# Optimization experiments

Hardware: AMD Instinct MI355X
Metric: run time of the kernel (lower is better)

The kernel has to match this reference:

```python
import jax, jax.numpy as jnp
import numpy as np

TOP_K = 48
NUM_RBF = 16
NUM_RBF_SC = 8
MAXREL = 32
EDGE_F = 128
EPS_D = 1e-6
LN_EPS = 1e-5


def gather_nodes(nodes, idx):
    # nodes: [B, L, C], idx: [B, L, K] -> [B, L, K, C]
    return jax.vmap(lambda n, i: n[i])(nodes, idx)


def rbf(D, count):
    # D: [..., ] -> [..., count]; mu in [2, 22], sigma = 20/count
    mu = jnp.linspace(2.0, 22.0, count)
    sigma = (22.0 - 2.0) / count
    return jnp.exp(-(((D[..., None] - mu) / sigma) ** 2))


def layer_norm(x, g, b):
    mu = jnp.mean(x, -1, keepdims=True)
    var = jnp.mean((x - mu) ** 2, -1, keepdims=True)
    return g * (x - mu) / jnp.sqrt(var + LN_EPS) + b


def setup_inputs() -> dict:
    key = jax.random.key(0)
    ks = jax.random.split(key, 8)
    B, Lr = 1, 1024
    X = jax.random.normal(ks[0], (B, Lr, 37, 3), dtype=jnp.float32)
    mask = jnp.ones((B, Lr), dtype=jnp.float32)
    atom_mask = jnp.ones((B, Lr, 37), dtype=jnp.float32)
    residue_idx = jnp.arange(B * Lr, dtype=jnp.int64 if jax.config.jax_enable_x64 else jnp.int32).reshape(B, Lr)
    dihedral_mask = jnp.ones((B, Lr), dtype=jnp.float32)
    chain_labels = jnp.zeros((B, Lr), dtype=jnp.int32)
    W_pos = jax.random.normal(ks[1], (16, 2 * MAXREL + 2), dtype=jnp.float32) * 0.1
    b_pos = jnp.zeros((16,), dtype=jnp.float32)
    W_e = jax.random.normal(ks[2], (EDGE_F, 16 + NUM_RBF * 25), dtype=jnp.float32) * 0.05
    g_e = jnp.ones((EDGE_F,), dtype=jnp.float32)
    be_e = jnp.zeros((EDGE_F,), dtype=jnp.float32)
    W_s = jax.random.normal(ks[3], (EDGE_F, NUM_RBF_SC * 32 * 5), dtype=jnp.float32) * 0.05
    g_s = jnp.ones((EDGE_F,), dtype=jnp.float32)
    b_s = jnp.zeros((EDGE_F,), dtype=jnp.float32)
    return {"X": X, "L": 1024, "mask": mask, "atom_mask": atom_mask,
            "residue_idx": residue_idx, "dihedral_mask": dihedral_mask,
            "chain_labels": chain_labels, "W_pos": W_pos, "b_pos": b_pos,
            "W_e": W_e, "g_e": g_e, "be_e": be_e, "W_s": W_s, "g_s": g_s, "b_s": b_s}


def reference(X, L, mask, atom_mask, residue_idx, dihedral_mask, chain_labels,
              W_pos, b_pos, W_e, g_e, be_e, W_s, g_s, b_s):
    # Virtual Cb from ideal geometry
    b_v = X[:, :, 1, :] - X[:, :, 0, :]
    c_v = X[:, :, 2, :] - X[:, :, 1, :]
    a_v = jnp.cross(b_v, c_v)
    Cb = -0.58273431 * a_v + 0.56802827 * b_v - 0.54067466 * c_v + X[:, :, 1, :]
    Ca = X[:, :, 1, :]
    N = X[:, :, 0, :]
    C = X[:, :, 2, :]
    O = X[:, :, 4, :]

    # _dist: masked pairwise Ca distances + top-k smallest
    mask2d = mask[:, None, :] * mask[:, :, None]  # [B, L, L]
    dX = Ca[:, :, None, :] - Ca[:, None, :, :]
    D = mask2d * jnp.sqrt(jnp.sum(dX ** 2, -1) + EPS_D)
    D_max = jnp.max(D, -1, keepdims=True)
    D_adj = D + (1.0 - mask2d) * D_max
    neg_vals, E_idx = jax.lax.top_k(-D_adj, TOP_K)
    D_neighbors = -neg_vals  # [B, L, K]

    coords = {'N': N, 'Ca': Ca, 'C': C, 'O': O, 'Cb': Cb}
    pairs = [('N','N'),('C','C'),('O','O'),('Cb','Cb'),('Ca','N'),('Ca','C'),('Ca','O'),
             ('Ca','Cb'),('N','C'),('N','O'),('N','Cb'),('Cb','C'),('Cb','O'),('O','C'),
             ('N','Ca'),('C','Ca'),('O','Ca'),('Cb','Ca'),('C','N'),('O','N'),('Cb','N'),
             ('C','Cb'),('O','Cb'),('C','O')]
    A_st = jnp.stack([coords[a] for a, _ in pairs])  # [24, B, L, 3]
    B_st = jnp.stack([coords[b] for _, b in pairs])
    B_nb = jax.vmap(gather_nodes, (0, None))(B_st, E_idx)  # [24, B, L, K, 3]
    Dp = jnp.sqrt(jnp.sum((A_st[:, :, :, None, :] - B_nb) ** 2, -1) + EPS_D)  # [24,B,L,K]
    RBF_pairs = rbf(Dp, NUM_RBF)  # [24, B, L, K, 16]
    Bt, Lr, K = E_idx.shape
    RBF_pairs = jnp.moveaxis(RBF_pairs, 0, 3).reshape(Bt, Lr, K, 24 * NUM_RBF)
    RBF_all = jnp.concatenate([rbf(D_neighbors, NUM_RBF), RBF_pairs], -1)  # [B,L,K,400]

    # Positional encodings
    ri_nb = gather_nodes(residue_idx[..., None], E_idx)[..., 0]  # [B,L,K]
    offset = residue_idx[:, :, None] - ri_nb
    ch_nb = gather_nodes(chain_labels[..., None], E_idx)[..., 0]
    E_chains = (chain_labels[:, :, None] - ch_nb == 0).astype(jnp.int32)
    d = jnp.clip(offset + MAXREL, 0, 2 * MAXREL) * E_chains + (1 - E_chains) * (2 * MAXREL + 1)
    d_onehot = jax.nn.one_hot(d, 2 * MAXREL + 2, dtype=jnp.float32)
    E_positional = d_onehot @ W_pos.T + b_pos
    E = jnp.concatenate([E_positional, RBF_all], -1)  # [B,L,K,416]

    # Sidechain RBFs on the first min(100, K) neighbors
    Ks = min(100, K)
    E_idx_sub = E_idx[:, :, :Ks]
    am_g = gather_nodes(atom_mask, E_idx_sub)  # [B,L,Ks,37]
    S = X[:, :, 5:37, :]  # [B,L,32,3]
    S_nb = gather_nodes(S.reshape(Bt, Lr, 32 * 3), E_idx_sub).reshape(Bt, Lr, Ks, 32, 3)
    anchors = jnp.stack([N, Ca, C, O, Cb], 2)  # [B,L,5,3], anchor order matches loop order
    Ds = jnp.sqrt(jnp.sum((anchors[:, :, None, :, None, :] - S_nb[:, :, :, None, :, :]) ** 2, -1) + EPS_D)
    # Ds: [B,L,Ks,5,32]; rbf_side -> [B,L,Ks,5,32,8]; masked by neighbor atom mask
    RBF_s = rbf(Ds, NUM_RBF_SC) * am_g[:, :, :, None, 5:37, None]
    E_s = RBF_s.reshape(Bt, Lr, Ks, 5 * 32 * NUM_RBF_SC)  # [B,L,Ks,1280]

    E_s = layer_norm(E_s @ W_s.T, g_s, b_s)
    E = layer_norm(E @ W_e.T, g_e, be_e)
    return (E, E_idx, E_s, E_idx_sub)
```

## Files before the change

### kernel.cpp

```cpp
#include <hip/hip_runtime.h>
#include <math.h>

#define LRES 1024
#define TOPK 48
#define NEDGE (LRES*TOPK)

typedef short short8 __attribute__((ext_vector_type(8)));
typedef float f32x4  __attribute__((ext_vector_type(4)));

#define OUT_E     0
#define OUT_EIDX  6291456
#define OUT_ES    6340608
#define OUT_EIDX2 12632064

#define WS_COORDS 0
#define WS_DNB    15360
#define WS_EIDX   64512
#define WS_WPE    113664
#define WS_WPS    140288

#define DE 1.06666667f
#define QE 0.10273976f
#define DS 1.14285714f
#define QS 0.07337053f

__constant__ int PA[24] = {0,2,3,4,1,1,1,1,0,0,0,4,4,3,0,2,3,4,2,3,4,2,3,2};
__constant__ int PB[24] = {0,2,3,4,0,2,3,4,2,3,4,2,3,2,1,1,1,1,0,0,0,4,4,3};

__device__ inline short f2bf(float f) {
    unsigned u = __float_as_uint(f);
    unsigned r = (u + 0x7FFFu + ((u >> 16) & 1u)) >> 16;
    return (short)r;
}

__device__ inline short8 pack8(const float* fv) {
    union { short8 s; unsigned u[4]; } r;
    #pragma unroll
    for (int i = 0; i < 4; ++i)
        r.u[i] = __builtin_amdgcn_perm(__float_as_uint(fv[2*i+1]),
                                       __float_as_uint(fv[2*i]), 0x07060302u);
    return r.s;
}

template<int MT>
__device__ __forceinline__ void kred_ln(const f32x4 (*acc)[8], float* hb,
                                        float* outp, const float* g,
                                        const float* b, int t, int w,
                                        int quad, int l16) {
    int e = t >> 4, c = t & 15;
    float gv[8], bv[8];
    #pragma unroll
    for (int k = 0; k < 8; ++k) { gv[k] = g[c + 16*k]; bv[k] = b[c + 16*k]; }
    float* hw = hb + w*2144;
    #pragma unroll
    for (int mt = 0; mt < MT; ++mt) {
        __syncthreads();
        #pragma unroll
        for (int nt = 0; nt < 8; ++nt)
        #pragma unroll
        for (int r = 0; r < 4; ++r)
            hw[(quad*4 + r)*134 + nt*16 + l16] = acc[mt][nt][r];
        __syncthreads();
        float s = 0.f, s2 = 0.f, vals[8];
        #pragma unroll
        for (int k = 0; k < 8; ++k) {
            int col = e*134 + c + 16*k;
            float v = hb[col] + hb[2144 + col] + hb[4288 + col] + hb[6432 + col];
            vals[k] = v; s += v; s2 = fmaf(v, v, s2);
        }
        #pragma unroll
        for (int m = 1; m <= 8; m <<= 1) {
            s  += __shfl_xor(s,  m);
            s2 += __shfl_xor(s2, m);
        }
        float mu = s * 0.0078125f;
        float rs = rsqrtf(fmaf(s2, 0.0078125f, -mu*mu) + 1e-5f);
        float* row = outp + (size_t)(mt*16 + e)*128 + c;
        #pragma unroll
        for (int k = 0; k < 8; ++k)
            __builtin_nontemporal_store(gv[k]*(vals[k] - mu)*rs + bv[k],
                                        &row[16*k]);
    }
}

__global__ __launch_bounds__(256) void k_pre(const float* __restrict__ X,
                                             const float* __restrict__ mask,
                                             const float* __restrict__ We,
                                             const float* __restrict__ Ws,
                                             float* __restrict__ coords,
                                             short* __restrict__ WpE,
                                             short* __restrict__ WpS,
                                             float* __restrict__ Dnb,
                                             int* __restrict__ Eidx,
                                             float* __restrict__ out) {
    int blk = blockIdx.x, t = threadIdx.x;
    if (blk < 256) {
        __shared__ float sCa[LRES*3];
        __shared__ float sM[LRES];
        for (int j = t; j < LRES; j += 256) {
            sCa[j*3+0] = X[j*111 + 3];
            sCa[j*3+1] = X[j*111 + 4];
            sCa[j*3+2] = X[j*111 + 5];
            sM[j] = mask[j];
        }
        __syncthreads();
        int w = t >> 6, lane = t & 63;
        int i = blk * 4 + w;
        float cx = sCa[i*3], cy = sCa[i*3+1], cz = sCa[i*3+2];
        float mi = sM[i];
        float dv[16], m2v[16];
        float lmax = -1e30f;
        #pragma unroll
        for (int s = 0; s < 16; ++s) {
            int j = s*64 + lane;
            float dx = cx - sCa[j*3], dy = cy - sCa[j*3+1], dz = cz - sCa[j*3+2];
            float d  = __builtin_amdgcn_sqrtf(dx*dx + dy*dy + dz*dz + 1e-6f);
            float m2 = mi * sM[j];
            dv[s] = m2 * d; m2v[s] = m2;
            lmax = fmaxf(lmax, dv[s]);
        }
        #pragma unroll
        for (int off = 32; off; off >>= 1) lmax = fmaxf(lmax, __shfl_xor(lmax, off));
        unsigned long long key[16];
        unsigned long long mkey = ~0ull; int mslot = 0;
        #pragma unroll
        for (int s = 0; s < 16; ++s) {
            float dadj = dv[s] + (1.0f - m2v[s]) * lmax;
            key[s] = (((unsigned long long)__float_as_uint(dadj)) << 10) | (unsigned)(s*64 + lane);
            if (key[s] < mkey) { mkey = key[s]; mslot = s; }
        }
        for (int it = 0; it < TOPK; ++it) {
            unsigned long long wk = mkey;
            #pragma unroll
            for (int off = 32; off; off >>= 1) {
                unsigned long long o = __shfl_xor(wk, off);
                wk = (o < wk) ? o : wk;
            }
            if (lane == 0) {
                int j = (int)(wk & 1023u);
                int id = i*TOPK + it;
                Dnb[id]  = __uint_as_float((unsigned)(wk >> 10));
                Eidx[id] = j;
                out[OUT_EIDX  + id] = (float)j;
                out[OUT_EIDX2 + id] = (float)j;
            }
            if (mkey == wk) {
                key[mslot] = ~0ull;
                mkey = ~0ull;
                #pragma unroll
                for (int s = 0; s < 16; ++s)
                    if (key[s] < mkey) { mkey = key[s]; mslot = s; }
            }
        }
    } else if (blk < 896) {
        int g = (blk - 256) * 256 + t;
        if (g < 8*13*64*8) {
            int j = g & 7, lane = (g >> 3) & 63, gg = g >> 9;
            int ks = gg % 13, nt = gg / 13;
            int n = nt*16 + (lane & 15), k = ks*32 + (lane >> 4)*8 + j;
            WpE[g] = f2bf(We[n*416 + k]);
        }
        if (g < 8*40*64*8) {
            int j = g & 7, lane = (g >> 3) & 63, gg = g >> 9;
            int ks = gg % 40, nt = gg / 40;
            int n = nt*16 + (lane & 15), k = ks*32 + (lane >> 4)*8 + j;
            WpS[g] = f2bf(Ws[n*1280 + k]);
        }
    } else {
        int r = (blk - 896) * 256 + t;
        if (r >= LRES) return;
        const float* xr = X + r * 111;
        float N[3], Ca[3], C[3], O[3], bv[3], cv[3], av[3];
        #pragma unroll
        for (int d = 0; d < 3; ++d) {
            N[d]  = xr[0*3 + d];  Ca[d] = xr[1*3 + d];
            C[d]  = xr[2*3 + d];  O[d]  = xr[4*3 + d];
            bv[d] = Ca[d] - N[d]; cv[d] = C[d] - Ca[d];
        }
        av[0] = bv[1]*cv[2] - bv[2]*cv[1];
        av[1] = bv[2]*cv[0] - bv[0]*cv[2];
        av[2] = bv[0]*cv[1] - bv[1]*cv[0];
        float* o = coords + r * 15;
        #pragma unroll
        for (int d = 0; d < 3; ++d) {
            float Cb = -0.58273431f*av[d] + 0.56802827f*bv[d] - 0.54067466f*cv[d] + Ca[d];
            o[0*3+d] = N[d]; o[1*3+d] = Ca[d]; o[2*3+d] = C[d];
            o[3*3+d] = O[d]; o[4*3+d] = Cb;
        }
    }
}

__global__ __launch_bounds__(256, 2) void k_edge(const float* __restrict__ coords,
                                                 const float* __restrict__ X,
                                                 const float* __restrict__ amask,
                                                 const short* __restrict__ WpE,
                                                 const short* __restrict__ WpS,
                                                 const float* __restrict__ Dnb,
                                                 const int* __restrict__ Eidx,
                                                 const int* __restrict__ ri,
                                                 const int* __restrict__ ch,
                                                 const float* __restrict__ Wpos,
                                                 const float* __restrict__ bpos,
                                                 const float* __restrict__ ge,
                                                 const float* __restrict__ be,
                                                 const float* __restrict__ gs,
                                                 const float* __restrict__ bs,
                                                 float* __restrict__ out) {
    __shared__ float smem[8624];
    int t = threadIdx.x;
    int w = t >> 6, lane = t & 63, quad = lane >> 4, l16 = lane & 15;
    float* hb = smem;

    if (blockIdx.x < 768) {
        float* sA3 = smem + 8576;
        int id0 = blockIdx.x * 64;
        int i0 = id0 / TOPK;

        if (t < 30) {
            int rr = i0 + t / 15;
            if (rr > LRES-1) rr = LRES-1;
            sA3[t] = coords[rr*15 + t%15];
        }
        int s1 = 4*w + quad;
        float S[4][2][3], am[4][2];
        int im[4];
        #pragma unroll
        for (int mt = 0; mt < 4; ++mt) {
            int id = id0 + mt*16 + l16;
            int j  = Eidx[id];
            im[mt] = id / TOPK;
            const float* xp = X + (j*37 + 5)*3;
            const float* ap = amask + j*37 + 5;
            #pragma unroll
            for (int h = 0; h < 2; ++h) {
                int s = s1 + h*16;
                S[mt][h][0] = xp[s*3+0];
                S[mt][h][1] = xp[s*3+1];
                S[mt][h][2] = xp[s*3+2];
                am[mt][h]   = ap[s];
            }
        }
        __syncthreads();

        f32x4 acc[4][8] = {};
        const short8* bp = (const short8*)WpS;

        for (int a = 0; a < 5; ++a) {
            float A[4][3];
            #pragma unroll
            for (int mt = 0; mt < 4; ++mt) {
                int base = (im[mt] - i0)*15 + a*3;
                A[mt][0] = sA3[base+0];
                A[mt][1] = sA3[base+1];
                A[mt][2] = sA3[base+2];
            }
            #pragma unroll
            for (int h = 0; h < 2; ++h) {
                int ks = a*8 + w + h*4;
                short8 afrag[4];
                #pragma unroll
                for (int mt = 0; mt < 4; ++mt) {
                    float dx = A[mt][0] - S[mt][h][0];
                    float dy = A[mt][1] - S[mt][h][1];
                    float dz = A[mt][2] - S[mt][h][2];
                    float d  = __builtin_amdgcn_sqrtf(fmaf(dz,dz,fmaf(dy,dy,fmaf(dx,dx,1e-6f))));
                    float u  = fmaf(d, 0.4f, -0.8f);
                    float e0 = __expf(-u*u) * am[mt][h];
                    float g  = __expf(fmaf(2.0f*DS, u, -DS*DS));
                    float fv[8];
                    fv[0] = e0;
                    #pragma unroll
                    for (int r = 1; r < 8; ++r) { e0 *= g; g *= QS; fv[r] = e0; }
                    afrag[mt] = pack8(fv);
                }
                #pragma unroll
                for (int nt = 0; nt < 8; ++nt) {
                    short8 b = bp[(nt*40 + ks)*64 + lane];
                    acc[0][nt] = __builtin_amdgcn_mfma_f32_16x16x32_bf16(afrag[0], b, acc[0][nt], 0,0,0);
                    acc[1][nt] = __builtin_amdgcn_mfma_f32_16x16x32_bf16(afrag[1], b, acc[1][nt], 0,0,0);
                    acc[2][nt] = __builtin_amdgcn_mfma_f32_16x16x32_bf16(afrag[2], b, acc[2][nt], 0,0,0);
                    acc[3][nt] = __builtin_amdgcn_mfma_f32_16x16x32_bf16(afrag[3], b, acc[3][nt], 0,0,0);
                }
            }
        }
        kred_ln<4>(acc, hb, out + OUT_ES + (size_t)id0*128, gs, bs, t, w, quad, l16);
    } else {
        float* sdist = hb;
        float* sposf = hb + 1728;
        int*   sdpos = (int*)(hb + 2816);
        float* sA    = hb + 2880;
        float* sB    = hb + 3840;
        int id0 = (blockIdx.x - 768) * 64;

        if (t < 64) {
            int id = id0 + t, i = id / TOPK, j = Eidx[id];
            int off = ri[i] - ri[j];
            sdpos[t] = (ch[i] == ch[j]) ? min(max(off + 32, 0), 64) : 65;
            sdist[t*27] = Dnb[id];
        }
        for (int it = t; it < 64*15; it += 256) {
            int e = it / 15, q = it % 15;
            int id = id0 + e, i = id / TOPK, j = Eidx[id];
            sA[e*15+q] = coords[i*15+q];
            sB[e*15+q] = coords[j*15+q];
        }
        __syncthreads();
        for (int it = t; it < 64*24; it += 256) {
            int e = it / 24, p = it % 24, a = PA[p], b = PB[p];
            float dx = sA[e*15+a*3+0] - sB[e*15+b*3+0];
            float dy = sA[e*15+a*3+1] - sB[e*15+b*3+1];
            float dz = sA[e*15+a*3+2] - sB[e*15+b*3+2];
            sdist[e*27 + 1 + p] = __builtin_amdgcn_sqrtf(dx*dx + dy*dy + dz*dz + 1e-6f);
        }
        for (int it = t; it < 64*16; it += 256) {
            int e = it >> 4, c = it & 15;
            sposf[e*17 + c] = Wpos[c*66 + sdpos[e]] + bpos[c];
        }
        __syncthreads();

        f32x4 acc[4][8] = {};
        const short8* bp = (const short8*)WpE;
        float rb = (quad & 1) ? 8.0f*DE : 0.0f;

        for (int ks = w; ks < 13; ks += 4) {
            short8 afrag[4];
            #pragma unroll
            for (int mt = 0; mt < 4; ++mt) {
                int e = mt*16 + l16;
                float fv[8];
                if (ks == 0 && quad < 2) {
                    #pragma unroll
                    for (int j = 0; j < 8; ++j) fv[j] = sposf[e*17 + quad*8 + j];
                } else {
                    int p = (ks == 0) ? 0 : (2*ks - 1 + (quad >> 1));
                    float d = sdist[e*27 + p];
                    float u = fmaf(d, 0.8f, -1.6f) - rb;
                    float e0 = __expf(-u*u);
                    float g  = __expf(fmaf(2.0f*DE, u, -DE*DE));
                    fv[0] = e0;
                    #pragma unroll
                    for (int r = 1; r < 8; ++r) { e0 *= g; g *= QE; fv[r] = e0; }
                }
                afrag[mt] = pack8(fv);
            }
            #pragma unroll
            for (int nt = 0; nt < 8; ++nt) {
                short8 b = bp[(nt*13 + ks)*64 + lane];
                acc[0][nt] = __builtin_amdgcn_mfma_f32_16x16x32_bf16(afrag[0], b, acc[0][nt], 0,0,0);
                acc[1][nt] = __builtin_amdgcn_mfma_f32_16x16x32_bf16(afrag[1], b, acc[1][nt], 0,0,0);
                acc[2][nt] = __builtin_amdgcn_mfma_f32_16x16x32_bf16(afrag[2], b, acc[2][nt], 0,0,0);
                acc[3][nt] = __builtin_amdgcn_mfma_f32_16x16x32_bf16(afrag[3], b, acc[3][nt], 0,0,0);
            }
        }
        kred_ln<4>(acc, hb, out + OUT_E + (size_t)id0*128, ge, be, t, w, quad, l16);
    }
}

extern "C" void kernel_launch(void* const* d_in, const int* in_sizes, int n_in,
                              void* d_out, int out_size, void* d_ws, size_t ws_size,
                              hipStream_t stream) {
    (void)in_sizes; (void)n_in; (void)out_size; (void)ws_size;
    const float* X     = (const float*)d_in[0];
    const float* mask  = (const float*)d_in[2];
    const float* amask = (const float*)d_in[3];
    const int*   ri    = (const int*)d_in[4];
    const int*   ch    = (const int*)d_in[6];
    const float* Wpos  = (const float*)d_in[7];
    const float* bpos  = (const float*)d_in[8];
    const float* We    = (const float*)d_in[9];
    const float* ge    = (const float*)d_in[10];
    const float* be    = (const float*)d_in[11];
    const float* Ws    = (const float*)d_in[12];
    const float* gs    = (const float*)d_in[13];
    const float* bs    = (const float*)d_in[14];

    float* out    = (float*)d_out;
    float* ws     = (float*)d_ws;
    float* coords = ws + WS_COORDS;
    float* Dnb    = ws + WS_DNB;
    int*   Eidx   = (int*)(ws + WS_EIDX);
    short* WpE    = (short*)(ws + WS_WPE);
    short* WpS    = (short*)(ws + WS_WPS);

    k_pre <<<dim3(900),  dim3(256), 0, stream>>>(X, mask, We, Ws, coords,
                                                 WpE, WpS, Dnb, Eidx, out);
    k_edge<<<dim3(1536), dim3(256), 0, stream>>>(coords, X, amask, WpE, WpS,
                                                 Dnb, Eidx, ri, ch, Wpos, bpos,
                                                 ge, be, gs, bs, out);
}
```

Measured before the change: 181.6 us.

## Double-buffer weight fragments into LDS via async global_load_lds prefetch

New measurement: 183.5 us. Within noise of the previous version (+1.0%).

```diff
diff --git a/kernel.cpp b/kernel.cpp
--- a/kernel.cpp
+++ b/kernel.cpp
@@ -7,6 +7,7 @@
 
 typedef short short8 __attribute__((ext_vector_type(8)));
 typedef float f32x4  __attribute__((ext_vector_type(4)));
+typedef unsigned int u32;
 
 #define OUT_E     0
 #define OUT_EIDX  6291456
@@ -41,6 +42,17 @@
                                        __float_as_uint(fv[2*i]), 0x07060302u);
     return r.s;
 }
+
+__device__ __forceinline__ void gload16(const void* g, void* l) {
+    __builtin_amdgcn_global_load_lds(
+        (const __attribute__((address_space(1))) u32*)g,
+        (__attribute__((address_space(3))) u32*)l, 16, 0, 0);
+}
+
+#define WAIT_VM(N) do {                                             \
+    asm volatile("s_waitcnt vmcnt(" #N ")" ::: "memory");           \
+    __builtin_amdgcn_sched_barrier(0);                              \
+} while (0)
 
 template<int MT>
 __device__ __forceinline__ void kred_ln(const f32x4 (*acc)[8], float* hb,
@@ -206,13 +218,14 @@
                                                  const float* __restrict__ gs,
                                                  const float* __restrict__ bs,
                                                  float* __restrict__ out) {
-    __shared__ float smem[8624];
+    __shared__ __align__(16) short sStage[4][2][4096];
+    __shared__ float sScr[2880];
     int t = threadIdx.x;
     int w = t >> 6, lane = t & 63, quad = lane >> 4, l16 = lane & 15;
-    float* hb = smem;
+    float* hb = (float*)sStage;
 
     if (blockIdx.x < 768) {
-        float* sA3 = smem + 8576;
+        float* sA3 = sScr;
         int id0 = blockIdx.x * 64;
         int i0 = id0 / TOPK;
 
@@ -242,54 +255,57 @@
         }
         __syncthreads();
 
+        const short* wsrc = (const short*)WpS;
+        #pragma unroll
+        for (int nt = 0; nt < 8; ++nt)
+            gload16(wsrc + (nt*40 + w)*512 + lane*8, &sStage[w][0][nt*512]);
+
         f32x4 acc[4][8] = {};
-        const short8* bp = (const short8*)WpS;
-
-        for (int a = 0; a < 5; ++a) {
-            float A[4][3];
+        #pragma unroll
+        for (int p = 0; p < 10; ++p) {
+            if (p < 9) {
+                int ksn = w + 4*(p+1);
+                #pragma unroll
+                for (int nt = 0; nt < 8; ++nt)
+                    gload16(wsrc + (nt*40 + ksn)*512 + lane*8,
+                            &sStage[w][(p+1)&1][nt*512]);
+            }
+            int a = p >> 1, h = p & 1;
+            short8 afrag[4];
             #pragma unroll
             for (int mt = 0; mt < 4; ++mt) {
                 int base = (im[mt] - i0)*15 + a*3;
-                A[mt][0] = sA3[base+0];
-                A[mt][1] = sA3[base+1];
-                A[mt][2] = sA3[base+2];
-            }
-            #pragma unroll
-            for (int h = 0; h < 2; ++h) {
-                int ks = a*8 + w + h*4;
-                short8 afrag[4];
+                float dx = sA3[base+0] - S[mt][h][0];
+                float dy = sA3[base+1] - S[mt][h][1];
+                float dz = sA3[base+2] - S[mt][h][2];
+                float d  = __builtin_amdgcn_sqrtf(fmaf(dz,dz,fmaf(dy,dy,fmaf(dx,dx,1e-6f))));
+                float u  = fmaf(d, 0.4f, -0.8f);
+                float e0 = __expf(-u*u) * am[mt][h];
+                float g  = __expf(fmaf(2.0f*DS, u, -DS*DS));
+                float fv[8];
+                fv[0] = e0;
                 #pragma unroll
-                for (int mt = 0; mt < 4; ++mt) {
-                    float dx = A[mt][0] - S[mt][h][0];
-                    float dy = A[mt][1] - S[mt][h][1];
-                    float dz = A[mt][2] - S[mt][h][2];
-                    float d  = __builtin_amdgcn_sqrtf(fmaf(dz,dz,fmaf(dy,dy,fmaf(dx,dx,1e-6f))));
-                    float u  = fmaf(d, 0.4f, -0.8f);
-                    float e0 = __expf(-u*u) * am[mt][h];
-                    float g  = __expf(fmaf(2.0f*DS, u, -DS*DS));
-                    float fv[8];
-                    fv[0] = e0;
-                    #pragma unroll
-                    for (int r = 1; r < 8; ++r) { e0 *= g; g *= QS; fv[r] = e0; }
-                    afrag[mt] = pack8(fv);
-                }
-                #pragma unroll
-                for (int nt = 0; nt < 8; ++nt) {
-                    short8 b = bp[(nt*40 + ks)*64 + lane];
-                    acc[0][nt] = __builtin_amdgcn_mfma_f32_16x16x32_bf16(afrag[0], b, acc[0][nt], 0,0,0);
-                    acc[1][nt] = __builtin_amdgcn_mfma_f32_16x16x32_bf16(afrag[1], b, acc[1][nt], 0,0,0);
-                    acc[2][nt] = __builtin_amdgcn_mfma_f32_16x16x32_bf16(afrag[2], b, acc[2][nt], 0,0,0);
-                    acc[3][nt] = __builtin_amdgcn_mfma_f32_16x16x32_bf16(afrag[3], b, acc[3][nt], 0,0,0);
-                }
+                for (int r = 1; r < 8; ++r) { e0 *= g; g *= QS; fv[r] = e0; }
+                afrag[mt] = pack8(fv);
+            }
+            if (p < 9) WAIT_VM(8); else WAIT_VM(0);
+            const short8* bb = (const short8*)&sStage[w][p&1][0];
+            #pragma unroll
+            for (int nt = 0; nt < 8; ++nt) {
+                short8 b = bb[nt*64 + lane];
+                acc[0][nt] = __builtin_amdgcn_mfma_f32_16x16x32_bf16(afrag[0], b, acc[0][nt], 0,0,0);
+                acc[1][nt] = __builtin_amdgcn_mfma_f32_16x16x32_bf16(afrag[1], b, acc[1][nt], 0,0,0);
+                acc[2][nt] = __builtin_amdgcn_mfma_f32_16x16x32_bf16(afrag[2], b, acc[2][nt], 0,0,0);
+                acc[3][nt] = __builtin_amdgcn_mfma_f32_16x16x32_bf16(afrag[3], b, acc[3][nt], 0,0,0);
             }
         }
         kred_ln<4>(acc, hb, out + OUT_ES + (size_t)id0*128, gs, bs, t, w, quad, l16);
     } else {
-        float* sdist = hb;
-        float* sposf = hb + 1728;
-        int*   sdpos = (int*)(hb + 2816);
-        float* sA    = hb + 2880;
-        float* sB    = hb + 3840;
+        float* sdist = sScr;
+        float* sposf = sScr + 1728;
+        int*   sdpos = (int*)(sScr + 2816);
+        float* sA    = (float*)sStage;
+        float* sB    = (float*)sStage + 960;
         int id0 = (blockIdx.x - 768) * 64;
 
         if (t < 64) {
@@ -306,11 +322,11 @@
         }
         __syncthreads();
         for (int it = t; it < 64*24; it += 256) {
-            int e = it / 24, p = it % 24, a = PA[p], b = PB[p];
+            int e = it / 24, pp = it % 24, a = PA[pp], b = PB[pp];
             float dx = sA[e*15+a*3+0] - sB[e*15+b*3+0];
             float dy = sA[e*15+a*3+1] - sB[e*15+b*3+1];
             float dz = sA[e*15+a*3+2] - sB[e*15+b*3+2];
-            sdist[e*27 + 1 + p] = __builtin_amdgcn_sqrtf(dx*dx + dy*dy + dz*dz + 1e-6f);
+            sdist[e*27 + 1 + pp] = __builtin_amdgcn_sqrtf(dx*dx + dy*dy + dz*dz + 1e-6f);
         }
         for (int it = t; it < 64*16; it += 256) {
             int e = it >> 4, c = it & 15;
@@ -318,11 +334,24 @@
         }
         __syncthreads();
 
+        const short* wsrc = (const short*)WpE;
+        int nP = (w == 0) ? 4 : 3;
+        #pragma unroll
+        for (int nt = 0; nt < 8; ++nt)
+            gload16(wsrc + (nt*13 + w)*512 + lane*8, &sStage[w][0][nt*512]);
+
         f32x4 acc[4][8] = {};
-        const short8* bp = (const short8*)WpE;
         float rb = (quad & 1) ? 8.0f*DE : 0.0f;
-
-        for (int ks = w; ks < 13; ks += 4) {
+        #pragma unroll 1
+        for (int p = 0; p < nP; ++p) {
+            int ks = w + 4*p;
+            if (p + 1 < nP) {
+                int ksn = ks + 4;
+                #pragma unroll
+                for (int nt = 0; nt < 8; ++nt)
+                    gload16(wsrc + (nt*13 + ksn)*512 + lane*8,
+                            &sStage[w][(p+1)&1][nt*512]);
+            }
             short8 afrag[4];
             #pragma unroll
             for (int mt = 0; mt < 4; ++mt) {
@@ -332,8 +361,8 @@
                     #pragma unroll
                     for (int j = 0; j < 8; ++j) fv[j] = sposf[e*17 + quad*8 + j];
                 } else {
-                    int p = (ks == 0) ? 0 : (2*ks - 1 + (quad >> 1));
-                    float d = sdist[e*27 + p];
+                    int pp = (ks == 0) ? 0 : (2*ks - 1 + (quad >> 1));
+                    float d = sdist[e*27 + pp];
                     float u = fmaf(d, 0.8f, -1.6f) - rb;
                     float e0 = __expf(-u*u);
                     float g  = __expf(fmaf(2.0f*DE, u, -DE*DE));
@@ -343,9 +372,11 @@
                 }
                 afrag[mt] = pack8(fv);
             }
+            if (p + 1 < nP) WAIT_VM(8); else WAIT_VM(0);
+            const short8* bb = (const short8*)&sStage[w][p&1][0];
             #pragma unroll
             for (int nt = 0; nt < 8; ++nt) {
-                short8 b = bp[(nt*13 + ks)*64 + lane];
+                short8 b = bb[nt*64 + lane];
                 acc[0][nt] = __builtin_amdgcn_mfma_f32_16x16x32_bf16(afrag[0], b, acc[0][nt], 0,0,0);
                 acc[1][nt] = __builtin_amdgcn_mfma_f32_16x16x32_bf16(afrag[1], b, acc[1][nt], 0,0,0);
                 acc[2][nt] = __builtin_amdgcn_mfma_f32_16x16x32_bf16(afrag[2], b, acc[2][nt], 0,0,0);
```
